# Kernel tuning notes

Measured on AMD Instinct MI355X. Metric: run time of the kernel, lower is better.

Reference implementation:

```python
import jax, jax.numpy as jnp
import numpy as np

L, D, H, FF, I, MAXREL = 6, 512, 8, 2048, 50, 128
HD = D // H
NREL = 2 * MAXREL + 1
EPS = 1e-5


def setup_inputs() -> dict:
    key = jax.random.key(0)
    ks = jax.random.split(key, 32)
    s = 0.02
    p = {
        'x': jax.random.normal(ks[0], (16, 512, I), dtype=jnp.float32),
        'in_w': jax.random.normal(ks[1], (I, D)) * s,
        'in_b': jnp.zeros((D,), jnp.float32),
        'Wq': jax.random.normal(ks[2], (L, D, D)) * s,
        'Wk': jax.random.normal(ks[3], (L, D, D)) * s,
        'Wv': jax.random.normal(ks[4], (L, D, D)) * s,
        'Wo': jax.random.normal(ks[5], (L, D, D)) * s,
        'bo': jnp.zeros((L, D), jnp.float32),
        'rel_emb': jax.random.normal(ks[6], (L, NREL, HD)) * s,
        'w1': jax.random.normal(ks[7], (L, D, FF)) * s,
        'b1': jnp.zeros((L, FF), jnp.float32),
        'w2': jax.random.normal(ks[8], (L, FF, D)) * s,
        'b2': jnp.zeros((L, D), jnp.float32),
        'ln1_g': jnp.ones((L, D), jnp.float32),
        'ln1_b': jnp.zeros((L, D), jnp.float32),
        'ln2_g': jnp.ones((L, D), jnp.float32),
        'ln2_b': jnp.zeros((L, D), jnp.float32),
        'on_g': jnp.ones((D,), jnp.float32),
        'on_b': jnp.zeros((D,), jnp.float32),
        'p1_w': jax.random.normal(ks[9], (D, D // 2)) * s,
        'p1_b': jnp.zeros((D // 2,), jnp.float32),
        'p2_w': jax.random.normal(ks[10], (D // 2, 1)) * s,
        'p2_b': jnp.zeros((1,), jnp.float32),
    }
    return p


def _layer_norm(x, g, b):
    m = jnp.mean(x, axis=-1, keepdims=True)
    v = jnp.mean(jnp.square(x - m), axis=-1, keepdims=True)
    return (x - m) * jax.lax.rsqrt(v + EPS) * g + b


def _sinusoidal_pe(seq_len, d_model):
    pos = jnp.arange(seq_len, dtype=jnp.float32)[:, None]
    div = jnp.exp(jnp.arange(0, d_model, 2, dtype=jnp.float32) * (-jnp.log(10000.0) / d_model))
    pe = jnp.zeros((seq_len, d_model), jnp.float32)
    pe = pe.at[:, 0::2].set(jnp.sin(pos * div))
    pe = pe.at[:, 1::2].set(jnp.cos(pos * div))
    return pe


def reference(x, in_w, in_b, Wq, Wk, Wv, Wo, bo, rel_emb, w1, b1, w2, b2,
              ln1_g, ln1_b, ln2_g, ln2_b, on_g, on_b, p1_w, p1_b, p2_w, p2_b):
    B, S, _ = x.shape
    scale = jnp.sqrt(jnp.float32(HD))
    # relative position index matrix [S, S] in [0, 2*MAXREL]
    r = jnp.arange(S)
    rel_idx = jnp.clip(r[None, :] - r[:, None], -MAXREL, MAXREL) + MAXREL

    h = x @ in_w + in_b                       # [B,S,D]
    h = h + _sinusoidal_pe(S, D)

    for l in range(L):
        q = (h @ Wq[l]).reshape(B, S, H, HD).transpose(0, 2, 1, 3)  # [B,H,S,hd]
        k = (h @ Wk[l]).reshape(B, S, H, HD).transpose(0, 2, 1, 3)
        v = (h @ Wv[l]).reshape(B, S, H, HD).transpose(0, 2, 1, 3)
        scores = jnp.einsum('bhqd,bhkd->bhqk', q, k) / scale
        rel = rel_emb[l][rel_idx]             # [S,S,hd]
        scores = scores + jnp.einsum('bhqd,qkd->bhqk', q, rel)  # rel bias is NOT scaled (matches source)
        attn = jax.nn.softmax(scores, axis=-1)
        ctx = jnp.einsum('bhqk,bhkd->bhqd', attn, v)
        ctx = ctx.transpose(0, 2, 1, 3).reshape(B, S, D)
        attn_out = ctx @ Wo[l] + bo[l]
        h = _layer_norm(h + attn_out, ln1_g[l], ln1_b[l])
        ff = jax.nn.relu(h @ w1[l] + b1[l]) @ w2[l] + b2[l]
        h = _layer_norm(h + ff, ln2_g[l], ln2_b[l])

    h = _layer_norm(h, on_g, on_b)
    out = jax.nn.relu(h @ p1_w + p1_b) @ p2_w + p2_b  # [B,S,1]
    return out
```

## Files before the change

### kernel.cpp

```cpp
#include <hip/hip_runtime.h>

typedef unsigned short u16;
typedef unsigned int   u32;
typedef short   short8  __attribute__((ext_vector_type(8)));
typedef float   floatx4 __attribute__((ext_vector_type(4)));

#define NTOK 8192
#define SEQ  512
#define NLAYER 6

#define OFF_WT   ((size_t)0)
#define OFF_HF   ((size_t)38010880)
#define OFF_HB   ((size_t)54788096)
#define OFF_QKV  ((size_t)63176704)
#define OFF_CTX  ((size_t)88342528)
#define OFF_GOUT ((size_t)96731136)
#define OFF_FF   ((size_t)113508352)
#define OFF_HD1  ((size_t)147062784)
#define OFF_VT   OFF_FF
#define OFF_RELB OFF_HD1

#define LSTRIDE 3145728
#define P1T_OFF 18874368

__device__ __forceinline__ float b2f(u16 v) { return __uint_as_float(((u32)v) << 16); }
__device__ __forceinline__ float lo16(u32 v) { return __uint_as_float(v << 16); }
__device__ __forceinline__ float hi16(u32 v) { return __uint_as_float(v & 0xffff0000u); }
__device__ __forceinline__ u16 f2b(float f) {
  u32 x = __float_as_uint(f);
  return (u16)((x + 0x7fffu + ((x >> 16) & 1u)) >> 16);
}
__device__ __forceinline__ u32 pack2(float a, float b) {
  return (u32)f2b(a) | ((u32)f2b(b) << 16);
}

typedef __attribute__((address_space(1))) void* gas_t;
typedef __attribute__((address_space(3))) void* las_t;

__global__ __launch_bounds__(256) void transpose_all(
    const float* __restrict__ Wq, const float* __restrict__ Wk,
    const float* __restrict__ Wv, const float* __restrict__ Wo,
    const float* __restrict__ w1, const float* __restrict__ w2,
    const float* __restrict__ p1, u16* __restrict__ wT)
{
  __shared__ u16 tile[64][65];
  const int tb = blockIdx.x;
  const float* src; u16* dst; int R, C, tidx;
  if (tb < 4608) {
    const int l = tb / 768, r = tb % 768;
    const size_t lofs = (size_t)l * LSTRIDE;
    if (r < 256) {
      const int m = r >> 6; tidx = r & 63; R = 512; C = 512;
      const float* bases[4] = {Wq, Wk, Wv, Wo};
      src = bases[m] + (size_t)l * 262144;
      dst = wT + lofs + (size_t)m * 262144;
    } else if (r < 512) {
      tidx = r - 256; R = 512; C = 2048;
      src = w1 + (size_t)l * 1048576; dst = wT + lofs + 1048576;
    } else {
      tidx = r - 512; R = 2048; C = 512;
      src = w2 + (size_t)l * 1048576; dst = wT + lofs + 2097152;
    }
  } else {
    tidx = tb - 4608; R = 512; C = 256;
    src = p1; dst = wT + P1T_OFF;
  }
  const int tcn = C >> 6;
  const int tr = tidx / tcn, tc = tidx % tcn;
  const int th = threadIdx.x;
  {
    const int lr = th >> 2, cg = (th & 3) * 16;
    const float* sp = src + (size_t)(tr*64 + lr) * C + tc*64 + cg;
    float4 f0 = *(const float4*)(sp);
    float4 f1 = *(const float4*)(sp + 4);
    float4 f2 = *(const float4*)(sp + 8);
    float4 f3 = *(const float4*)(sp + 12);
    u16* tp = &tile[lr][cg];
    tp[0]=f2b(f0.x); tp[1]=f2b(f0.y); tp[2]=f2b(f0.z); tp[3]=f2b(f0.w);
    tp[4]=f2b(f1.x); tp[5]=f2b(f1.y); tp[6]=f2b(f1.z); tp[7]=f2b(f1.w);
    tp[8]=f2b(f2.x); tp[9]=f2b(f2.y); tp[10]=f2b(f2.z); tp[11]=f2b(f2.w);
    tp[12]=f2b(f3.x); tp[13]=f2b(f3.y); tp[14]=f2b(f3.z); tp[15]=f2b(f3.w);
  }
  __syncthreads();
  {
    const int oc = th >> 2, rg = (th & 3) * 16;
    u32 wds[8];
    #pragma unroll
    for (int i = 0; i < 8; ++i)
      wds[i] = (u32)tile[rg + 2*i][oc] | ((u32)tile[rg + 2*i + 1][oc] << 16);
    u16* dp = dst + (size_t)(tc*64 + oc) * R + tr*64 + rg;
    uint4 o0; o0.x=wds[0]; o0.y=wds[1]; o0.z=wds[2]; o0.w=wds[3];
    uint4 o1; o1.x=wds[4]; o1.y=wds[5]; o1.z=wds[6]; o1.w=wds[7];
    *(uint4*)dp = o0;
    *(uint4*)(dp + 8) = o1;
  }
}

__global__ __launch_bounds__(128) void input_proj(
    const float* __restrict__ x, const float* __restrict__ w, const float* __restrict__ ib,
    float* __restrict__ hf, u16* __restrict__ hb)
{
  const int row = blockIdx.x, t = threadIdx.x;
  const int s = row & (SEQ - 1);
  __shared__ float xs[50];
  if (t < 50) xs[t] = x[row*50 + t];
  __syncthreads();
  #pragma unroll
  for (int rep = 0; rep < 4; ++rep) {
    const int d = rep*128 + t;
    float acc = ib[d];
    #pragma unroll
    for (int i = 0; i < 50; ++i) acc += xs[i] * w[i*512 + d];
    const int ii = d >> 1;
    const float dv = __expf((float)(2*ii) * -0.017988946f);
    const float ang = (float)s * dv;
    const float pe = (d & 1) ? cosf(ang) : sinf(ang);
    const float v = acc + pe;
    hf[(size_t)row*512 + d] = v;
    hb[(size_t)row*512 + d] = f2b(v);
  }
}

__global__ __launch_bounds__(256) void gemm_bt(
    const u16* __restrict__ A, const u16* __restrict__ Bt,
    const float* __restrict__ bias,
    float* __restrict__ outF0, float* __restrict__ outF1, u16* __restrict__ outB,
    u16* __restrict__ vTout,
    const int M, const int N, const int K, const int kLen, const int flags)
{
  __shared__ __align__(16) u16 As[2*128*32];
  __shared__ __align__(16) u16 Bs[2*128*32];
  const int nb = N >> 7;
  const int bm = blockIdx.x / nb, bn = blockIdx.x % nb;
  const int z = blockIdx.y;
  const int kOff = z * kLen;
  const int m0 = bm << 7, n0 = bn << 7;
  const int tid = threadIdx.x;
  const int wave = tid >> 6, lane = tid & 63;
  const int wr = (wave >> 1) << 6, wc = (wave & 1) << 6;
  const int lrow = lane & 15, lquad = lane >> 4;

  floatx4 acc[4][4];
  #pragma unroll
  for (int i = 0; i < 4; ++i)
    #pragma unroll
    for (int j = 0; j < 4; ++j) { floatx4 zz = {0.f,0.f,0.f,0.f}; acc[i][j] = zz; }

  const u16* a0p = A  + (size_t)m0 * K + kOff;
  const u16* b0p = Bt + (size_t)n0 * K + kOff;
  const int c0 = tid, c1 = 256 + tid;
  const int ar0 = c0 >> 2, as0 = (c0 & 3) * 8;
  const int ar1 = c1 >> 2, as1 = (c1 & 3) * 8;

  for (int k0 = 0; k0 < kLen; k0 += 64) {
    #pragma unroll
    for (int hh = 0; hh < 2; ++hh) {
      const int kk = k0 + hh*32;
      __builtin_amdgcn_global_load_lds((gas_t)(a0p + (size_t)ar0*K + kk + as0), (las_t)(&As[hh*4096 + c0*8]), 16, 0, 0);
      __builtin_amdgcn_global_load_lds((gas_t)(a0p + (size_t)ar1*K + kk + as1), (las_t)(&As[hh*4096 + c1*8]), 16, 0, 0);
      __builtin_amdgcn_global_load_lds((gas_t)(b0p + (size_t)ar0*K + kk + as0), (las_t)(&Bs[hh*4096 + c0*8]), 16, 0, 0);
      __builtin_amdgcn_global_load_lds((gas_t)(b0p + (size_t)ar1*K + kk + as1), (las_t)(&Bs[hh*4096 + c1*8]), 16, 0, 0);
    }
    __syncthreads();
    #pragma unroll
    for (int hh = 0; hh < 2; ++hh) {
      short8 af[4], bf[4];
      #pragma unroll
      for (int i = 0; i < 4; ++i) af[i] = *(const short8*)&As[hh*4096 + (wr + i*16 + lrow)*32 + lquad*8];
      #pragma unroll
      for (int j = 0; j < 4; ++j) bf[j] = *(const short8*)&Bs[hh*4096 + (wc + j*16 + lrow)*32 + lquad*8];
      #pragma unroll
      for (int i = 0; i < 4; ++i)
        #pragma unroll
        for (int j = 0; j < 4; ++j)
          acc[i][j] = __builtin_amdgcn_mfma_f32_16x16x32_bf16(af[i], bf[j], acc[i][j], 0, 0, 0);
    }
    __syncthreads();
  }

  if ((flags & 4) && n0 >= 1024) {
    #pragma unroll
    for (int j = 0; j < 4; ++j) {
      const int cm = (n0 - 1024) + wc + j*16 + lrow;
      const int hh = cm >> 6, d = cm & 63;
      #pragma unroll
      for (int i = 0; i < 4; ++i) {
        const int r0 = m0 + wr + i*16 + lquad*4;
        const int bb = r0 >> 9, s = r0 & 511;
        uint2 o;
        o.x = pack2(acc[i][j][0], acc[i][j][1]);
        o.y = pack2(acc[i][j][2], acc[i][j][3]);
        *(uint2*)(vTout + ((size_t)(bb*8 + hh)*64 + d)*512 + s) = o;
      }
    }
    return;
  }

  float* outF = (z == 0) ? outF0 : outF1;
  const bool hasb = ((flags & 1) != 0) && (z == 0);
  const bool dorelu = (flags & 2) != 0;
  #pragma unroll
  for (int j = 0; j < 4; ++j) {
    const int col = n0 + wc + j*16 + lrow;
    const float bv = hasb ? bias[col] : 0.f;
    #pragma unroll
    for (int i = 0; i < 4; ++i) {
      const int r0 = m0 + wr + i*16 + lquad*4;
      #pragma unroll
      for (int v = 0; v < 4; ++v) {
        float val = acc[i][j][v] + bv;
        if (dorelu) val = fmaxf(val, 0.f);
        const size_t off = (size_t)(r0 + v) * N + col;
        if (outB) outB[off] = f2b(val);
        else      outF[off] = val;
      }
    }
  }
}

__global__ __launch_bounds__(256) void cvt_rel_all(
    const float* __restrict__ rel, u16* __restrict__ relB)
{
  const int i = blockIdx.x*256 + threadIdx.x;
  if (i < 6*257*64) {
    const int l = i / 16448, rem = i % 16448;
    relB[l*17408 + rem] = f2b(rel[i]);
  }
}

__global__ __launch_bounds__(256) void attn_mfma(
    const u16* __restrict__ qkv, const u16* __restrict__ vT,
    const u16* __restrict__ relB, u16* __restrict__ ctx)
{
  const int id = blockIdx.x;
  const int xcd = id & 7, g = (id >> 3) & 15, qt = id >> 7;
  const int bh = xcd*16 + g;
  const int b = bh >> 3, h = bh & 7;
  const int t = threadIdx.x, w = t >> 6, lane = t & 63;
  const int lr = lane & 15, quad = lane >> 4;

  __shared__ __align__(16) u16 Ks[64*72];
  __shared__ __align__(16) u16 Vs[64*72];
  __shared__ __align__(16) u16 Pr[64*280];

  const size_t token0 = (size_t)b*512 + qt*64;

  short8 af0, af1;
  {
    const u16* qp = qkv + (token0 + w*16 + lr)*1536 + h*64 + quad*8;
    af0 = *(const short8*)(qp);
    af1 = *(const short8*)(qp + 32);
  }

  #pragma unroll 4
  for (int nt = 0; nt < 17; ++nt) {
    const u16* rp = relB + (nt*16 + lr)*64 + quad*8;
    short8 rb0 = *(const short8*)(rp);
    short8 rb1 = *(const short8*)(rp + 32);
    floatx4 c = {0.f,0.f,0.f,0.f};
    c = __builtin_amdgcn_mfma_f32_16x16x32_bf16(af0, rb0, c, 0, 0, 0);
    c = __builtin_amdgcn_mfma_f32_16x16x32_bf16(af1, rb1, c, 0, 0, 0);
    #pragma unroll
    for (int r = 0; r < 4; ++r)
      Pr[(w*16 + quad*4 + r)*280 + nt*16 + lr] = f2b(c[r]);
  }

  floatx4 oacc[4];
  floatx4 lacc = {0.f,0.f,0.f,0.f};
  #pragma unroll
  for (int n = 0; n < 4; ++n) { floatx4 zz = {0.f,0.f,0.f,0.f}; oacc[n] = zz; }

  short8 ones;
  #pragma unroll
  for (int i = 0; i < 8; ++i) ones[i] = (short)0x3F80;

  const int srow = t >> 2, scol = (t & 3) * 16;
  const u16* kbase = qkv + (size_t)b*512*1536 + 512 + h*64;
  const u16* vbase = vT + (size_t)(b*8 + h)*64*512;
  const int qg0 = qt*64 + w*16 + quad*4;

  uint4 kr0, kr1, vr0, vr1;
  {
    const u16* kp = kbase + (size_t)(srow)*1536 + scol;
    kr0 = *(const uint4*)kp; kr1 = *(const uint4*)(kp + 8);
    const u16* vp = vbase + (size_t)srow*512 + scol;
    vr0 = *(const uint4*)vp; vr1 = *(const uint4*)(vp + 8);
  }

  for (int kt = 0; kt < 8; ++kt) {
    __syncthreads();
    *(uint4*)&Ks[srow*72 + scol]     = kr0;
    *(uint4*)&Ks[srow*72 + scol + 8] = kr1;
    *(uint4*)&Vs[srow*72 + scol]     = vr0;
    *(uint4*)&Vs[srow*72 + scol + 8] = vr1;
    if (kt < 7) {
      const u16* kp = kbase + (size_t)((kt+1)*64 + srow)*1536 + scol;
      kr0 = *(const uint4*)kp; kr1 = *(const uint4*)(kp + 8);
      const u16* vp = vbase + (size_t)srow*512 + (kt+1)*64 + scol;
      vr0 = *(const uint4*)vp; vr1 = *(const uint4*)(vp + 8);
    }
    __syncthreads();

    floatx4 s4[4];
    #pragma unroll
    for (int nt = 0; nt < 4; ++nt) {
      short8 kb0 = *(const short8*)&Ks[(nt*16 + lr)*72 + quad*8];
      short8 kb1 = *(const short8*)&Ks[(nt*16 + lr)*72 + 32 + quad*8];
      floatx4 c = {0.f,0.f,0.f,0.f};
      c = __builtin_amdgcn_mfma_f32_16x16x32_bf16(af0, kb0, c, 0, 0, 0);
      c = __builtin_amdgcn_mfma_f32_16x16x32_bf16(af1, kb1, c, 0, 0, 0);
      s4[nt] = c;
    }
    __syncthreads();

    const int kpos = kt*64 + lr;
    #pragma unroll
    for (int r = 0; r < 4; ++r) {
      const int qg = qg0 + r;
      const int prrow = (w*16 + quad*4 + r)*280;
      const int psrow = (w*16 + quad*4 + r)*72;
      #pragma unroll
      for (int nt = 0; nt < 4; ++nt) {
        int dd = (kpos + nt*16) - qg;
        dd = dd < -128 ? -128 : (dd > 128 ? 128 : dd);
        const float sc = fmaf(s4[nt][r], 0.125f, b2f(Pr[prrow + dd + 128]));
        Ks[psrow + nt*16 + lr] = f2b(__expf(sc));
      }
    }

    short8 pf0 = *(const short8*)&Ks[(w*16 + lr)*72 + quad*8];
    short8 pf1 = *(const short8*)&Ks[(w*16 + lr)*72 + 32 + quad*8];
    lacc = __builtin_amdgcn_mfma_f32_16x16x32_bf16(pf0, ones, lacc, 0, 0, 0);
    lacc = __builtin_amdgcn_mfma_f32_16x16x32_bf16(pf1, ones, lacc, 0, 0, 0);
    #pragma unroll
    for (int nd = 0; nd < 4; ++nd) {
      short8 vb0 = *(const short8*)&Vs[(nd*16 + lr)*72 + quad*8];
      short8 vb1 = *(const short8*)&Vs[(nd*16 + lr)*72 + 32 + quad*8];
      oacc[nd] = __builtin_amdgcn_mfma_f32_16x16x32_bf16(pf0, vb0, oacc[nd], 0, 0, 0);
      oacc[nd] = __builtin_amdgcn_mfma_f32_16x16x32_bf16(pf1, vb1, oacc[nd], 0, 0, 0);
    }
  }

  #pragma unroll
  for (int r = 0; r < 4; ++r) {
    const float inv = 1.f / lacc[r];
    u16* cp = ctx + (token0 + w*16 + quad*4 + r)*512 + h*64 + lr;
    #pragma unroll
    for (int nd = 0; nd < 4; ++nd)
      cp[nd*16] = f2b(oacc[nd][r] * inv);
  }
}

__global__ __launch_bounds__(128) void ln_kernel(
    const float* __restrict__ res, const float* __restrict__ add0,
    const float* __restrict__ add1,
    const float* __restrict__ g, const float* __restrict__ be,
    float* __restrict__ hf, u16* __restrict__ hb)
{
  const int row = blockIdx.x, t = threadIdx.x;
  const size_t base = (size_t)row * 512;
  float4 x = *(const float4*)(res + base + t*4);
  if (add0) {
    const float4 a = *(const float4*)(add0 + base + t*4);
    x.x += a.x; x.y += a.y; x.z += a.z; x.w += a.w;
  }
  if (add1) {
    const float4 a = *(const float4*)(add1 + base + t*4);
    x.x += a.x; x.y += a.y; x.z += a.z; x.w += a.w;
  }
  float s = x.x + x.y + x.z + x.w;
  #pragma unroll
  for (int off = 32; off > 0; off >>= 1) s += __shfl_down(s, off);
  __shared__ float red[2];
  const int wv = t >> 6, ln = t & 63;
  if (ln == 0) red[wv] = s;
  __syncthreads();
  const float mean = (red[0] + red[1]) * (1.f/512.f);
  const float dx0 = x.x-mean, dx1 = x.y-mean, dx2 = x.z-mean, dx3 = x.w-mean;
  float vs = dx0*dx0 + dx1*dx1 + dx2*dx2 + dx3*dx3;
  __syncthreads();
  #pragma unroll
  for (int off = 32; off > 0; off >>= 1) vs += __shfl_down(vs, off);
  if (ln == 0) red[wv] = vs;
  __syncthreads();
  const float var = (red[0] + red[1]) * (1.f/512.f);
  const float inv = 1.f / sqrtf(var + 1e-5f);
  const float4 gv = *(const float4*)(g + t*4);
  const float4 bv = *(const float4*)(be + t*4);
  const float y0 = dx0*inv*gv.x + bv.x;
  const float y1 = dx1*inv*gv.y + bv.y;
  const float y2 = dx2*inv*gv.z + bv.z;
  const float y3 = dx3*inv*gv.w + bv.w;
  *(float4*)(hf + base + t*4) = make_float4(y0, y1, y2, y3);
  u32* hp = (u32*)(hb + base + t*4);
  hp[0] = pack2(y0, y1); hp[1] = pack2(y2, y3);
}

__global__ __launch_bounds__(256) void head2_kernel(
    const u16* __restrict__ hd1, const float* __restrict__ p2w,
    const float* __restrict__ p2b, float* __restrict__ out)
{
  const int wv = threadIdx.x >> 6, ln = threadIdx.x & 63;
  const int row = blockIdx.x * 4 + wv;
  const u16* hp = hd1 + (size_t)row * 256 + ln*4;
  const u32 h0 = *(const u32*)hp, h1 = *(const u32*)(hp + 2);
  const float4 w = *(const float4*)(p2w + ln*4);
  float acc = lo16(h0)*w.x + hi16(h0)*w.y + lo16(h1)*w.z + hi16(h1)*w.w;
  #pragma unroll
  for (int off = 1; off < 64; off <<= 1) acc += __shfl_xor(acc, off);
  if (ln == 0) out[row] = acc + p2b[0];
}

extern "C" void kernel_launch(void* const* d_in, const int* in_sizes, int n_in,
                              void* d_out, int out_size, void* d_ws, size_t ws_size,
                              hipStream_t stream) {
  (void)in_sizes; (void)n_in; (void)out_size; (void)ws_size;
  const float* X    = (const float*)d_in[0];
  const float* INW  = (const float*)d_in[1];
  const float* INB  = (const float*)d_in[2];
  const float* WQ   = (const float*)d_in[3];
  const float* WK   = (const float*)d_in[4];
  const float* WV   = (const float*)d_in[5];
  const float* WO   = (const float*)d_in[6];
  const float* BO   = (const float*)d_in[7];
  const float* REL  = (const float*)d_in[8];
  const float* W1   = (const float*)d_in[9];
  const float* B1   = (const float*)d_in[10];
  const float* W2   = (const float*)d_in[11];
  const float* B2   = (const float*)d_in[12];
  const float* LN1G = (const float*)d_in[13];
  const float* LN1B = (const float*)d_in[14];
  const float* LN2G = (const float*)d_in[15];
  const float* LN2B = (const float*)d_in[16];
  const float* ONG  = (const float*)d_in[17];
  const float* ONB  = (const float*)d_in[18];
  const float* P1W  = (const float*)d_in[19];
  const float* P1B  = (const float*)d_in[20];
  const float* P2W  = (const float*)d_in[21];
  const float* P2B  = (const float*)d_in[22];
  float* out = (float*)d_out;

  char* ws = (char*)d_ws;
  u16*   wT    = (u16*)(ws + OFF_WT);
  float* hF    = (float*)(ws + OFF_HF);
  u16*   hB    = (u16*)(ws + OFF_HB);
  u16*   qkv   = (u16*)(ws + OFF_QKV);
  u16*   ctx   = (u16*)(ws + OFF_CTX);
  float* gout0 = (float*)(ws + OFF_GOUT);
  float* gout1 = (float*)(ws + OFF_QKV);
  u16*   ff    = (u16*)(ws + OFF_FF);
  u16*   hd1   = (u16*)(ws + OFF_HD1);
  u16*   vTb   = (u16*)(ws + OFF_VT);
  u16*   relBa = (u16*)(ws + OFF_RELB);

  transpose_all<<<4640, 256, 0, stream>>>(WQ, WK, WV, WO, W1, W2, P1W, wT);
  cvt_rel_all<<<386, 256, 0, stream>>>(REL, relBa);
  input_proj<<<NTOK, 128, 0, stream>>>(X, INW, INB, hF, hB);

  for (int l = 0; l < NLAYER; ++l) {
    const u16* wTl = wT + (size_t)l * LSTRIDE;
    gemm_bt<<<dim3(768,1), 256, 0, stream>>>(hB, wTl, nullptr, nullptr, nullptr, qkv, vTb,
                                             8192, 1536, 512, 512, 4);
    attn_mfma<<<1024, 256, 0, stream>>>(qkv, vTb, relBa + l*17408, ctx);
    gemm_bt<<<dim3(256,2), 256, 0, stream>>>(ctx, wTl + 786432, BO + l*512,
                                             gout0, gout1, nullptr, nullptr,
                                             8192, 512, 512, 256, 1);
    ln_kernel<<<NTOK, 128, 0, stream>>>(hF, gout0, gout1, LN1G + l*512, LN1B + l*512, hF, hB);
    gemm_bt<<<dim3(1024,1), 256, 0, stream>>>(hB, wTl + 1048576, B1 + l*2048,
                                              nullptr, nullptr, ff, nullptr,
                                              8192, 2048, 512, 512, 3);
    gemm_bt<<<dim3(256,2), 256, 0, stream>>>(ff, wTl + 2097152, B2 + l*512,
                                             gout0, gout1, nullptr, nullptr,
                                             8192, 512, 2048, 1024, 1);
    ln_kernel<<<NTOK, 128, 0, stream>>>(hF, gout0, gout1, LN2G + l*512, LN2B + l*512, hF, hB);
  }
  ln_kernel<<<NTOK, 128, 0, stream>>>(hF, nullptr, nullptr, ONG, ONB, hF, hB);
  gemm_bt<<<dim3(128,1), 256, 0, stream>>>(hB, wT + P1T_OFF, P1B,
                                           nullptr, nullptr, hd1, nullptr,
                                           8192, 256, 512, 512, 3);
  head2_kernel<<<2048, 256, 0, stream>>>(hd1, P2W, P2B, out);
}
```

Before: 1.271 ms.

## Drop fp32 residual stream, swizzle GEMM blocks across XCDs, simplify attention loads

```diff
diff --git a/kernel.cpp b/kernel.cpp
--- a/kernel.cpp
+++ b/kernel.cpp
@@ -10,13 +10,12 @@
 #define NLAYER 6
 
 #define OFF_WT   ((size_t)0)
-#define OFF_HF   ((size_t)38010880)
-#define OFF_HB   ((size_t)54788096)
-#define OFF_QKV  ((size_t)63176704)
-#define OFF_CTX  ((size_t)88342528)
-#define OFF_GOUT ((size_t)96731136)
-#define OFF_FF   ((size_t)113508352)
-#define OFF_HD1  ((size_t)147062784)
+#define OFF_HB   ((size_t)38010880)
+#define OFF_QKV  ((size_t)46399488)
+#define OFF_CTX  ((size_t)71565312)
+#define OFF_GOUT ((size_t)79953920)
+#define OFF_FF   ((size_t)96731136)
+#define OFF_HD1  ((size_t)130285568)
 #define OFF_VT   OFF_FF
 #define OFF_RELB OFF_HD1
 
@@ -98,7 +97,7 @@
 
 __global__ __launch_bounds__(128) void input_proj(
     const float* __restrict__ x, const float* __restrict__ w, const float* __restrict__ ib,
-    float* __restrict__ hf, u16* __restrict__ hb)
+    u16* __restrict__ hb)
 {
   const int row = blockIdx.x, t = threadIdx.x;
   const int s = row & (SEQ - 1);
@@ -115,9 +114,7 @@
     const float dv = __expf((float)(2*ii) * -0.017988946f);
     const float ang = (float)s * dv;
     const float pe = (d & 1) ? cosf(ang) : sinf(ang);
-    const float v = acc + pe;
-    hf[(size_t)row*512 + d] = v;
-    hb[(size_t)row*512 + d] = f2b(v);
+    hb[(size_t)row*512 + d] = f2b(acc + pe);
   }
 }
 
@@ -131,7 +128,10 @@
   __shared__ __align__(16) u16 As[2*128*32];
   __shared__ __align__(16) u16 Bs[2*128*32];
   const int nb = N >> 7;
-  const int bm = blockIdx.x / nb, bn = blockIdx.x % nb;
+  const int id = blockIdx.x;
+  const int xcd = id & 7, rest = id >> 3;
+  const int bm = (rest & 7) * 8 + xcd;
+  const int bn = rest >> 3;
   const int z = blockIdx.y;
   const int kOff = z * kLen;
   const int m0 = bm << 7, n0 = bn << 7;
@@ -139,6 +139,7 @@
   const int wave = tid >> 6, lane = tid & 63;
   const int wr = (wave >> 1) << 6, wc = (wave & 1) << 6;
   const int lrow = lane & 15, lquad = lane >> 4;
+  (void)nb;
 
   floatx4 acc[4][4];
   #pragma unroll
@@ -279,25 +280,19 @@
   const u16* vbase = vT + (size_t)(b*8 + h)*64*512;
   const int qg0 = qt*64 + w*16 + quad*4;
 
-  uint4 kr0, kr1, vr0, vr1;
-  {
-    const u16* kp = kbase + (size_t)(srow)*1536 + scol;
-    kr0 = *(const uint4*)kp; kr1 = *(const uint4*)(kp + 8);
-    const u16* vp = vbase + (size_t)srow*512 + scol;
-    vr0 = *(const uint4*)vp; vr1 = *(const uint4*)(vp + 8);
-  }
-
   for (int kt = 0; kt < 8; ++kt) {
     __syncthreads();
-    *(uint4*)&Ks[srow*72 + scol]     = kr0;
-    *(uint4*)&Ks[srow*72 + scol + 8] = kr1;
-    *(uint4*)&Vs[srow*72 + scol]     = vr0;
-    *(uint4*)&Vs[srow*72 + scol + 8] = vr1;
-    if (kt < 7) {
-      const u16* kp = kbase + (size_t)((kt+1)*64 + srow)*1536 + scol;
-      kr0 = *(const uint4*)kp; kr1 = *(const uint4*)(kp + 8);
-      const u16* vp = vbase + (size_t)srow*512 + (kt+1)*64 + scol;
-      vr0 = *(const uint4*)vp; vr1 = *(const uint4*)(vp + 8);
+    {
+      const u16* kp = kbase + (size_t)(kt*64 + srow)*1536 + scol;
+      uint4 k0 = *(const uint4*)kp;
+      uint4 k1 = *(const uint4*)(kp + 8);
+      const u16* vp = vbase + (size_t)srow*512 + kt*64 + scol;
+      uint4 v0 = *(const uint4*)vp;
+      uint4 v1 = *(const uint4*)(vp + 8);
+      *(uint4*)&Ks[srow*72 + scol]     = k0;
+      *(uint4*)&Ks[srow*72 + scol + 8] = k1;
+      *(uint4*)&Vs[srow*72 + scol]     = v0;
+      *(uint4*)&Vs[srow*72 + scol + 8] = v1;
     }
     __syncthreads();
 
@@ -352,23 +347,25 @@
 }
 
 __global__ __launch_bounds__(128) void ln_kernel(
-    const float* __restrict__ res, const float* __restrict__ add0,
+    const u16* __restrict__ resB, const float* __restrict__ add0,
     const float* __restrict__ add1,
     const float* __restrict__ g, const float* __restrict__ be,
-    float* __restrict__ hf, u16* __restrict__ hb)
+    u16* __restrict__ hb)
 {
   const int row = blockIdx.x, t = threadIdx.x;
   const size_t base = (size_t)row * 512;
-  float4 x = *(const float4*)(res + base + t*4);
+  const u32 r0 = *(const u32*)(resB + base + t*4);
+  const u32 r1 = *(const u32*)(resB + base + t*4 + 2);
+  float x0 = lo16(r0), x1 = hi16(r0), x2 = lo16(r1), x3 = hi16(r1);
   if (add0) {
     const float4 a = *(const float4*)(add0 + base + t*4);
-    x.x += a.x; x.y += a.y; x.z += a.z; x.w += a.w;
+    x0 += a.x; x1 += a.y; x2 += a.z; x3 += a.w;
   }
   if (add1) {
     const float4 a = *(const float4*)(add1 + base + t*4);
-    x.x += a.x; x.y += a.y; x.z += a.z; x.w += a.w;
-  }
-  float s = x.x + x.y + x.z + x.w;
+    x0 += a.x; x1 += a.y; x2 += a.z; x3 += a.w;
+  }
+  float s = x0 + x1 + x2 + x3;
   #pragma unroll
   for (int off = 32; off > 0; off >>= 1) s += __shfl_down(s, off);
   __shared__ float red[2];
@@ -376,7 +373,7 @@
   if (ln == 0) red[wv] = s;
   __syncthreads();
   const float mean = (red[0] + red[1]) * (1.f/512.f);
-  const float dx0 = x.x-mean, dx1 = x.y-mean, dx2 = x.z-mean, dx3 = x.w-mean;
+  const float dx0 = x0-mean, dx1 = x1-mean, dx2 = x2-mean, dx3 = x3-mean;
   float vs = dx0*dx0 + dx1*dx1 + dx2*dx2 + dx3*dx3;
   __syncthreads();
   #pragma unroll
@@ -391,7 +388,6 @@
   const float y1 = dx1*inv*gv.y + bv.y;
   const float y2 = dx2*inv*gv.z + bv.z;
   const float y3 = dx3*inv*gv.w + bv.w;
-  *(float4*)(hf + base + t*4) = make_float4(y0, y1, y2, y3);
   u32* hp = (u32*)(hb + base + t*4);
   hp[0] = pack2(y0, y1); hp[1] = pack2(y2, y3);
 }
@@ -442,7 +438,6 @@
 
   char* ws = (char*)d_ws;
   u16*   wT    = (u16*)(ws + OFF_WT);
-  float* hF    = (float*)(ws + OFF_HF);
   u16*   hB    = (u16*)(ws + OFF_HB);
   u16*   qkv   = (u16*)(ws + OFF_QKV);
   u16*   ctx   = (u16*)(ws + OFF_CTX);
@@ -455,7 +450,7 @@
 
   transpose_all<<<4640, 256, 0, stream>>>(WQ, WK, WV, WO, W1, W2, P1W, wT);
   cvt_rel_all<<<386, 256, 0, stream>>>(REL, relBa);
-  input_proj<<<NTOK, 128, 0, stream>>>(X, INW, INB, hF, hB);
+  input_proj<<<NTOK, 128, 0, stream>>>(X, INW, INB, hB);
 
   for (int l = 0; l < NLAYER; ++l) {
     const u16* wTl = wT + (size_t)l * LSTRIDE;
@@ -465,16 +460,16 @@
     gemm_bt<<<dim3(256,2), 256, 0, stream>>>(ctx, wTl + 786432, BO + l*512,
                                              gout0, gout1, nullptr, nullptr,
                                              8192, 512, 512, 256, 1);
-    ln_kernel<<<NTOK, 128, 0, stream>>>(hF, gout0, gout1, LN1G + l*512, LN1B + l*512, hF, hB);
+    ln_kernel<<<NTOK, 128, 0, stream>>>(hB, gout0, gout1, LN1G + l*512, LN1B + l*512, hB);
     gemm_bt<<<dim3(1024,1), 256, 0, stream>>>(hB, wTl + 1048576, B1 + l*2048,
                                               nullptr, nullptr, ff, nullptr,
                                               8192, 2048, 512, 512, 3);
     gemm_bt<<<dim3(256,2), 256, 0, stream>>>(ff, wTl + 2097152, B2 + l*512,
                                              gout0, gout1, nullptr, nullptr,
                                              8192, 512, 2048, 1024, 1);
-    ln_kernel<<<NTOK, 128, 0, stream>>>(hF, gout0, gout1, LN2G + l*512, LN2B + l*512, hF, hB);
-  }
-  ln_kernel<<<NTOK, 128, 0, stream>>>(hF, nullptr, nullptr, ONG, ONB, hF, hB);
+    ln_kernel<<<NTOK, 128, 0, stream>>>(hB, gout0, gout1, LN2G + l*512, LN2B + l*512, hB);
+  }
+  ln_kernel<<<NTOK, 128, 0, stream>>>(hB, nullptr, nullptr, ONG, ONB, hB);
   gemm_bt<<<dim3(128,1), 256, 0, stream>>>(hB, wT + P1T_OFF, P1B,
                                            nullptr, nullptr, hd1, nullptr,
                                            8192, 256, 512, 512, 3);
```

New measurement: 1.219 ms. -4.1%, faster.
